# Optimization experiments

Hardware: AMD Instinct MI355X
Metric: run time of the kernel (lower is better)

Reference implementation:

```python
import jax, jax.numpy as jnp
import numpy as np

TEMPERATURE = 0.5
SCALE_BY_TEMPERATURE = True
CURV = 0.05

N = 8192
D = 128
N_PRIMARY = 32
N_SECONDARY = 16


def setup_inputs() -> dict:
    key = jax.random.key(0)
    k1, k2, k3 = jax.random.split(key, 3)
    features = jax.random.normal(k1, (N, D), dtype=jnp.float32)
    primary_labels = jax.random.randint(k2, (N,), 0, N_PRIMARY)
    secondary_labels = jax.random.randint(k3, (N,), 0, N_SECONDARY)
    return {"features": features, "primary_labels": primary_labels,
            "secondary_labels": secondary_labels}


def _hyp_contrastive_loss(features, primary_labels, secondary_labels):
    c = CURV
    sqrt_c = c ** 0.5
    n = features.shape[0]

    # L2 normalize (torch F.normalize with eps=1e-12)
    nrm = jnp.maximum(jnp.linalg.norm(features, axis=1, keepdims=True), 1e-12)
    f = features / nrm

    # Pairwise mobius_add(-f[j], f[i]) at [i, j]. With x = -f[j], y = f[i]:
    #   num = (1 + 2c<x,y> + c|y|^2) x + (1 - c|x|^2) y,   den = 1 + 2c<x,y> + c^2|x|^2|y|^2
    # We only need ||num||/den, so expand ||num||^2 algebraically to avoid an
    # [N, N, D] intermediate (same math, exact).
    n2 = jnp.sum(f * f, axis=1)            # [N], ~1 after normalize
    s = f @ f.T                            # [N, N] <f_i, f_j>
    xy = -s                                # <x, y>
    x2 = n2[None, :]                       # |x|^2 = |f_j|^2
    y2 = n2[:, None]                       # |y|^2 = |f_i|^2

    A = 1.0 + 2.0 * c * xy + c * y2
    B = 1.0 - c * x2
    den = jnp.maximum(1.0 + 2.0 * c * xy + c * c * x2 * y2, 1e-15)
    num_sq = jnp.maximum(A * A * x2 + 2.0 * A * B * xy + B * B * y2, 0.0)
    norm_diff = sqrt_c * jnp.sqrt(num_sq) / den           # [N, N]

    # artanh with clamp (pm.artanh clamps argument below 1)
    distance = jnp.arctanh(jnp.clip(norm_diff, 0.0, 1.0 - 1e-7)) * 2.0 / sqrt_c

    anchor_dot_contrast = -distance / TEMPERATURE
    logits_max = jax.lax.stop_gradient(
        jnp.max(anchor_dot_contrast, axis=1, keepdims=True))
    logits = anchor_dot_contrast - logits_max
    exp_logits = jnp.exp(logits)

    pmask = (primary_labels[:, None] == primary_labels[None, :]).astype(f.dtype)
    smask = (secondary_labels[:, None] == secondary_labels[None, :]).astype(f.dtype)
    combined = jnp.minimum(pmask + smask, 1.0)

    eye = jnp.eye(n, dtype=f.dtype)
    positives_mask = combined * (1.0 - eye)
    negatives_mask = 1.0 - combined

    num_pos = jnp.sum(positives_mask, axis=1)             # [N]
    valid = num_pos > 0

    pos_contrib = jnp.sum(exp_logits * positives_mask, axis=1)
    neg_contrib = jnp.sum(exp_logits * negatives_mask, axis=1)
    denominator = pos_contrib + neg_contrib + 1e-8        # [N]

    log_probs = logits - jnp.log(denominator)[:, None]
    row_sum = jnp.sum(log_probs * positives_mask, axis=1)
    per_row = jnp.where(valid, row_sum / jnp.maximum(num_pos, 1.0), 0.0)

    n_valid = jnp.sum(valid.astype(f.dtype))
    loss = -jnp.sum(per_row) / jnp.maximum(n_valid, 1.0)  # mean over valid rows
    loss = jnp.where(n_valid > 0, loss, 0.0)
    if SCALE_BY_TEMPERATURE:
        loss = loss * TEMPERATURE
    return jnp.nan_to_num(loss, nan=0.0, posinf=0.0, neginf=0.0)


def reference(features, primary_labels, secondary_labels):
    return _hyp_contrastive_loss(features, primary_labels, secondary_labels)
```

## Files before the change

### kernel.cpp

```cpp
#include <hip/hip_runtime.h>
#include <hip/hip_bf16.h>

#define NN 8192
#define DD 128

typedef short short8 __attribute__((ext_vector_type(8)));
typedef __bf16 bf16x8 __attribute__((ext_vector_type(8)));
typedef float f32x4 __attribute__((ext_vector_type(4)));
typedef float f32x2 __attribute__((ext_vector_type(2)));

#define MKc (-0.110803324099723f)
#define PKc (0.110803324099723f)
#define C1Kc (1.110803324099723f)
#define KEc (-8.944271909999159f)
#define KLc (-6.199696797323639f)

__global__ __launch_bounds__(256) void prep_kernel(const float* __restrict__ x,
                                                   __hip_bfloat16* __restrict__ fb,
                                                   float* __restrict__ totg,
                                                   float* __restrict__ tposg) {
  int r = threadIdx.x >> 4, sub = threadIdx.x & 15;
  int row = blockIdx.x * 16 + r;
  const float4 a = *(const float4*)(x + (size_t)row * DD + sub * 8);
  const float4 b = *(const float4*)(x + (size_t)row * DD + sub * 8 + 4);
  float ss = a.x * a.x + a.y * a.y + a.z * a.z + a.w * a.w +
             b.x * b.x + b.y * b.y + b.z * b.z + b.w * b.w;
  for (int off = 1; off < 16; off <<= 1) ss += __shfl_xor(ss, off, 16);
  float inv = 1.0f / fmaxf(sqrtf(ss), 1e-12f);
  float va[8] = {a.x, a.y, a.z, a.w, b.x, b.y, b.z, b.w};
  short8 h;
  for (int j = 0; j < 8; j++) {
    __hip_bfloat16 t = __float2bfloat16(va[j] * inv);
    h[j] = __builtin_bit_cast(short, t);
  }
  *(short8*)((short*)fb + (size_t)row * DD + sub * 8) = h;
  if (threadIdx.x < 16) {
    totg[blockIdx.x * 16 + threadIdx.x] = 0.f;
    tposg[blockIdx.x * 16 + threadIdx.x] = 0.f;
  }
}

__global__ __launch_bounds__(256, 2) void fused_kernel(
    const __hip_bfloat16* __restrict__ fbg,
    const int* __restrict__ plab, const int* __restrict__ slab,
    float* __restrict__ totg, float* __restrict__ tposg) {
  __shared__ int plc[512], slc[512];
  __shared__ float colT_l[4 * 512];
  __shared__ float colG_l[4 * 512];

  const int tid = threadIdx.x;
  const int w = tid >> 6;
  const int lane = tid & 63;
  const int lrow = lane & 15;
  const int quad = lane >> 4;

  int J = 0, rem = blockIdx.x;
  while (rem >= 64 - 4 * J) { rem -= 64 - 4 * J; J++; }
  const int I = 4 * J + rem;
  const bool needMask = (I < 4 * J + 4);
  const int R0 = I * 128;
  const int C0 = J * 512;

  for (int i = tid; i < 512; i += 256) {
    plc[i] = plab[C0 + i];
    slc[i] = slab[C0 + i];
  }
  for (int i = lane; i < 512; i += 64) {
    colT_l[w * 512 + i] = 0.f;
    colG_l[w * 512 + i] = 0.f;
  }

  bf16x8 af[2][4];
  int plr[2][4], slr[2][4];
  for (int strip = 0; strip < 2; strip++) {
    const short* fa = (const short*)fbg + (size_t)(R0 + w * 32 + strip * 16 + lrow) * DD;
    for (int kk = 0; kk < 4; kk++)
      af[strip][kk] = __builtin_bit_cast(bf16x8, *(const short8*)(fa + kk * 32 + quad * 8));
    for (int r = 0; r < 4; r++) {
      int rowg = R0 + w * 32 + strip * 16 + quad * 4 + r;
      plr[strip][r] = plab[rowg];
      slr[strip][r] = slab[rowg];
    }
  }
  __syncthreads();

  const f32x2 MK2 = {MKc, MKc}, PK2 = {PKc, PKc}, C1K2 = {C1Kc, C1Kc};
  const f32x2 KE2 = {KEc, KEc}, ZERO2 = {0.f, 0.f}, EPS2 = {1e-30f, 1e-30f};
  const f32x2 ONE2 = {1.f, 1.f};

  f32x2 t2[2][2], g2[2][2];
  for (int s_ = 0; s_ < 2; s_++)
    for (int p = 0; p < 2; p++) { t2[s_][p] = ZERO2; g2[s_][p] = ZERO2; }

  const short* bp = (const short*)fbg + (size_t)(C0 + lrow) * DD + quad * 8;
  int colg = C0 + lrow;

  for (int ct = 0; ct < 32; ct++) {
    bf16x8 bf[4];
    for (int kk = 0; kk < 4; kk++)
      bf[kk] = __builtin_bit_cast(bf16x8, *(const short8*)(bp + kk * 32));
    bp += 16 * DD;

    f32x4 acc[2];
    for (int strip = 0; strip < 2; strip++) {
      f32x4 a0 = {0.f, 0.f, 0.f, 0.f};
      for (int kk = 0; kk < 4; kk++)
        a0 = __builtin_amdgcn_mfma_f32_16x16x32_bf16(af[strip][kk], bf[kk], a0, 0, 0, 0);
      acc[strip] = a0;
    }

    const int lc = ct * 16 + lrow;
    const int pc = plc[lc];
    const int sc = slc[lc];

    f32x2 colE = ZERO2, colL = ZERO2;

    for (int strip = 0; strip < 2; strip++) {
      for (int p = 0; p < 2; p++) {
        f32x2 s2 = {acc[strip][2 * p], acc[strip][2 * p + 1]};
        f32x2 tK = __builtin_elementwise_fma(s2, MK2, PK2);
        tK = __builtin_elementwise_max(tK, ZERO2);
        f32x2 dk = __builtin_elementwise_fma(s2, MK2, C1K2);
        f32x2 m = __builtin_elementwise_max(tK * dk, EPS2);
        f32x2 rq = {__builtin_amdgcn_rsqf(m.x), __builtin_amdgcn_rsqf(m.y)};
        f32x2 nd = tK * rq;
        f32x2 p1 = nd + ONE2;
        f32x2 rr = p1 * p1 * dk;
        f32x2 lg = {__log2f(rr.x), __log2f(rr.y)};
        f32x2 el = KE2 * lg;
        f32x2 e = {exp2f(el.x), exp2f(el.y)};
        const int r0 = 2 * p, r1 = 2 * p + 1;
        bool same0 = (pc == plr[strip][r0]) || (sc == slr[strip][r0]);
        bool same1 = (pc == plr[strip][r1]) || (sc == slr[strip][r1]);
        f32x2 em, lm;
        if (needMask) {
          int rg0 = R0 + w * 32 + strip * 16 + quad * 4 + r0;
          bool ok0 = (colg < rg0);
          bool ok1 = (colg < rg0 + 1);
          em.x = ok0 ? e.x : 0.f;
          em.y = ok1 ? e.y : 0.f;
          lm.x = (same0 && ok0) ? lg.x : 0.f;
          lm.y = (same1 && ok1) ? lg.y : 0.f;
        } else {
          em = e;
          lm.x = same0 ? lg.x : 0.f;
          lm.y = same1 ? lg.y : 0.f;
        }
        t2[strip][p] += em;
        g2[strip][p] += lm;
        colE += em;
        colL += lm;
      }
    }

    float cE = colE.x + colE.y;
    float cL = colL.x + colL.y;
    cE += __shfl_xor(cE, 16, 64);
    cE += __shfl_xor(cE, 32, 64);
    cL += __shfl_xor(cL, 16, 64);
    cL += __shfl_xor(cL, 32, 64);
    if (quad == 0) {
      colT_l[w * 512 + lc] += cE;
      colG_l[w * 512 + lc] += cL;
    }
    colg += 16;
  }

  for (int strip = 0; strip < 2; strip++) {
    for (int r = 0; r < 4; r++) {
      float t = t2[strip][r >> 1][r & 1];
      float g = g2[strip][r >> 1][r & 1];
      for (int off = 1; off < 16; off <<= 1) {
        t += __shfl_xor(t, off, 16);
        g += __shfl_xor(g, off, 16);
      }
      if (lrow == 0) {
        int rowg = R0 + w * 32 + strip * 16 + quad * 4 + r;
        atomicAdd(&totg[rowg], t);
        atomicAdd(&tposg[rowg], g);
      }
    }
  }

  __syncthreads();
  for (int i = tid; i < 512; i += 256) {
    float sE = colT_l[i] + colT_l[512 + i] + colT_l[1024 + i] + colT_l[1536 + i];
    float sL = colG_l[i] + colG_l[512 + i] + colG_l[1024 + i] + colG_l[1536 + i];
    atomicAdd(&totg[C0 + i], sE);
    atomicAdd(&tposg[C0 + i], sL);
  }
}

__global__ __launch_bounds__(1024) void finalize_k(const float* __restrict__ totg,
                                                   const float* __restrict__ tposg,
                                                   const int* __restrict__ plab,
                                                   const int* __restrict__ slab,
                                                   float* __restrict__ out) {
  __shared__ int hist[512];
  __shared__ int cntP[32], cntS[16];
  __shared__ float redP[16], redV[16];
  const int tid = threadIdx.x;
  if (tid < 512) hist[tid] = 0;
  __syncthreads();
  for (int i = tid; i < NN; i += 1024)
    atomicAdd(&hist[plab[i] * 16 + slab[i]], 1);
  __syncthreads();
  if (tid < 32) {
    int s = 0;
    for (int j = 0; j < 16; j++) s += hist[tid * 16 + j];
    cntP[tid] = s;
  } else if (tid >= 64 && tid < 80) {
    int s = 0;
    for (int j = 0; j < 32; j++) s += hist[j * 16 + (tid - 64)];
    cntS[tid - 64] = s;
  }
  __syncthreads();
  float accP = 0.f, accV = 0.f;
  for (int i = tid; i < NN; i += 1024) {
    int pl = plab[i], sl = slab[i];
    int np = cntP[pl] + cntS[sl] - hist[pl * 16 + sl] - 1;
    if (np > 0) {
      accP += (KLc * tposg[i]) / (float)np - __logf(totg[i] + 1e-8f);
      accV += 1.f;
    }
  }
  for (int off = 32; off; off >>= 1) {
    accP += __shfl_xor(accP, off, 64);
    accV += __shfl_xor(accV, off, 64);
  }
  int wv = tid >> 6;
  if ((tid & 63) == 0) { redP[wv] = accP; redV[wv] = accV; }
  __syncthreads();
  if (tid == 0) {
    float sp = 0.f, sv = 0.f;
    for (int j = 0; j < 16; j++) { sp += redP[j]; sv += redV[j]; }
    float loss = -(sp / fmaxf(sv, 1.0f)) * 0.5f;
    if (sv <= 0.0f || !__builtin_isfinite(loss)) loss = 0.0f;
    out[0] = loss;
  }
}

extern "C" void kernel_launch(void* const* d_in, const int* in_sizes, int n_in,
                              void* d_out, int out_size, void* d_ws, size_t ws_size,
                              hipStream_t stream) {
  const float* x = (const float*)d_in[0];
  const int* pl = (const int*)d_in[1];
  const int* sl = (const int*)d_in[2];
  char* ws = (char*)d_ws;
  __hip_bfloat16* fb = (__hip_bfloat16*)ws;
  float* totg = (float*)(ws + 2097152);
  float* tposg = (float*)(ws + 2129920);

  prep_kernel<<<NN / 16, 256, 0, stream>>>(x, fb, totg, tposg);
  fused_kernel<<<544, 256, 0, stream>>>(fb, pl, sl, totg, tposg);
  finalize_k<<<1, 1024, 0, stream>>>(totg, tposg, pl, sl, (float*)d_out);
}
```

Before: 123.8 us.

## Balance triangular work by pairing row blocks u and 63-u across 512 blocks

Replaces the 544-block triangular tile schedule with 512 blocks. Each block handles an equal share (32 or 33 column tiles) of a paired row-block set (u and 63-u), split into up to two segments with per-tile diagonal masking. This is meant to even out per-block work and remove the tail caused by uneven triangular blocks. In exchange, labels are now read from global memory per column tile instead of from a shared-memory cache, and the per-tile mask check and segment bookkeeping add overhead.

```diff
diff --git a/kernel.cpp b/kernel.cpp
--- a/kernel.cpp
+++ b/kernel.cpp
@@ -44,9 +44,8 @@
     const __hip_bfloat16* __restrict__ fbg,
     const int* __restrict__ plab, const int* __restrict__ slab,
     float* __restrict__ totg, float* __restrict__ tposg) {
-  __shared__ int plc[512], slc[512];
-  __shared__ float colT_l[4 * 512];
-  __shared__ float colG_l[4 * 512];
+  __shared__ float colT_l[4 * 528];
+  __shared__ float colG_l[4 * 528];
 
   const int tid = threadIdx.x;
   const int w = tid >> 6;
@@ -54,140 +53,155 @@
   const int lrow = lane & 15;
   const int quad = lane >> 4;
 
-  int J = 0, rem = blockIdx.x;
-  while (rem >= 64 - 4 * J) { rem -= 64 - 4 * J; J++; }
-  const int I = 4 * J + rem;
-  const bool needMask = (I < 4 * J + 4);
-  const int R0 = I * 128;
-  const int C0 = J * 512;
-
-  for (int i = tid; i < 512; i += 256) {
-    plc[i] = plab[C0 + i];
-    slc[i] = slab[C0 + i];
-  }
-  for (int i = lane; i < 512; i += 64) {
-    colT_l[w * 512 + i] = 0.f;
-    colG_l[w * 512 + i] = 0.f;
-  }
-
-  bf16x8 af[2][4];
-  int plr[2][4], slr[2][4];
-  for (int strip = 0; strip < 2; strip++) {
-    const short* fa = (const short*)fbg + (size_t)(R0 + w * 32 + strip * 16 + lrow) * DD;
-    for (int kk = 0; kk < 4; kk++)
-      af[strip][kk] = __builtin_bit_cast(bf16x8, *(const short8*)(fa + kk * 32 + quad * 8));
-    for (int r = 0; r < 4; r++) {
-      int rowg = R0 + w * 32 + strip * 16 + quad * 4 + r;
-      plr[strip][r] = plab[rowg];
-      slr[strip][r] = slab[rowg];
-    }
-  }
-  __syncthreads();
+  const int u = blockIdx.x >> 4;
+  const int k = blockIdx.x & 15;
+  const int s = (k < 8) ? 33 * k : 32 * k + 8;
+  const int c = (k < 8) ? 33 : 32;
+  const int B = 8 * (u + 1);
+
+  const int aEnd = min(s + c, B);
+  const int aCnt = max(0, aEnd - s);
+  const int bStart = max(s, B);
+  const int bCnt = max(0, s + c - bStart);
+  int segR0[2], segCol[2], segCnt[2], segLds[2];
+  segR0[0] = 128 * u;        segCol[0] = s * 16;              segCnt[0] = aCnt; segLds[0] = 0;
+  segR0[1] = 128 * (63 - u); segCol[1] = (bStart - B) * 16;   segCnt[1] = bCnt; segLds[1] = aCnt;
+
+  for (int i = lane; i < 528; i += 64) {
+    colT_l[w * 528 + i] = 0.f;
+    colG_l[w * 528 + i] = 0.f;
+  }
 
   const f32x2 MK2 = {MKc, MKc}, PK2 = {PKc, PKc}, C1K2 = {C1Kc, C1Kc};
   const f32x2 KE2 = {KEc, KEc}, ZERO2 = {0.f, 0.f}, EPS2 = {1e-30f, 1e-30f};
   const f32x2 ONE2 = {1.f, 1.f};
 
-  f32x2 t2[2][2], g2[2][2];
-  for (int s_ = 0; s_ < 2; s_++)
-    for (int p = 0; p < 2; p++) { t2[s_][p] = ZERO2; g2[s_][p] = ZERO2; }
-
-  const short* bp = (const short*)fbg + (size_t)(C0 + lrow) * DD + quad * 8;
-  int colg = C0 + lrow;
-
-  for (int ct = 0; ct < 32; ct++) {
-    bf16x8 bf[4];
-    for (int kk = 0; kk < 4; kk++)
-      bf[kk] = __builtin_bit_cast(bf16x8, *(const short8*)(bp + kk * 32));
-    bp += 16 * DD;
-
-    f32x4 acc[2];
+  for (int seg = 0; seg < 2; seg++) {
+    const int cnt = segCnt[seg];
+    if (cnt == 0) continue;
+    const int R0 = segR0[seg];
+    const int colBase = segCol[seg];
+    const int ldsBase = segLds[seg];
+
+    bf16x8 af[2][4];
+    int plr[2][4], slr[2][4];
     for (int strip = 0; strip < 2; strip++) {
-      f32x4 a0 = {0.f, 0.f, 0.f, 0.f};
+      const short* fa = (const short*)fbg + (size_t)(R0 + w * 32 + strip * 16 + lrow) * DD;
       for (int kk = 0; kk < 4; kk++)
-        a0 = __builtin_amdgcn_mfma_f32_16x16x32_bf16(af[strip][kk], bf[kk], a0, 0, 0, 0);
-      acc[strip] = a0;
-    }
-
-    const int lc = ct * 16 + lrow;
-    const int pc = plc[lc];
-    const int sc = slc[lc];
-
-    f32x2 colE = ZERO2, colL = ZERO2;
+        af[strip][kk] = __builtin_bit_cast(bf16x8, *(const short8*)(fa + kk * 32 + quad * 8));
+      for (int r = 0; r < 4; r++) {
+        int rowg = R0 + w * 32 + strip * 16 + quad * 4 + r;
+        plr[strip][r] = plab[rowg];
+        slr[strip][r] = slab[rowg];
+      }
+    }
+
+    f32x2 t2[2][2], g2[2][2];
+    for (int s_ = 0; s_ < 2; s_++)
+      for (int p = 0; p < 2; p++) { t2[s_][p] = ZERO2; g2[s_][p] = ZERO2; }
+
+    const short* bp = (const short*)fbg + (size_t)(colBase + lrow) * DD + quad * 8;
+    int colg = colBase + lrow;
+
+    for (int ct = 0; ct < cnt; ct++) {
+      bf16x8 bf[4];
+      for (int kk = 0; kk < 4; kk++)
+        bf[kk] = __builtin_bit_cast(bf16x8, *(const short8*)(bp + kk * 32));
+      bp += 16 * DD;
+
+      f32x4 acc[2];
+      for (int strip = 0; strip < 2; strip++) {
+        f32x4 a0 = {0.f, 0.f, 0.f, 0.f};
+        for (int kk = 0; kk < 4; kk++)
+          a0 = __builtin_amdgcn_mfma_f32_16x16x32_bf16(af[strip][kk], bf[kk], a0, 0, 0, 0);
+        acc[strip] = a0;
+      }
+
+      const int pc = plab[colg];
+      const int sc = slab[colg];
+      const bool mct = (colg - lrow + 240 >= R0);
+      f32x2 colE = ZERO2, colL = ZERO2;
+
+      for (int strip = 0; strip < 2; strip++) {
+        for (int p = 0; p < 2; p++) {
+          f32x2 s2 = {acc[strip][2 * p], acc[strip][2 * p + 1]};
+          f32x2 tK = __builtin_elementwise_fma(s2, MK2, PK2);
+          tK = __builtin_elementwise_max(tK, ZERO2);
+          f32x2 dk = __builtin_elementwise_fma(s2, MK2, C1K2);
+          f32x2 m = __builtin_elementwise_max(tK * dk, EPS2);
+          f32x2 rq = {__builtin_amdgcn_rsqf(m.x), __builtin_amdgcn_rsqf(m.y)};
+          f32x2 nd = tK * rq;
+          f32x2 p1 = nd + ONE2;
+          f32x2 rr = p1 * p1 * dk;
+          f32x2 lg = {__log2f(rr.x), __log2f(rr.y)};
+          f32x2 el = KE2 * lg;
+          f32x2 e = {exp2f(el.x), exp2f(el.y)};
+          const int r0 = 2 * p, r1 = 2 * p + 1;
+          bool same0 = (pc == plr[strip][r0]) || (sc == slr[strip][r0]);
+          bool same1 = (pc == plr[strip][r1]) || (sc == slr[strip][r1]);
+          f32x2 em, lm;
+          if (mct) {
+            int rg0 = R0 + w * 32 + strip * 16 + quad * 4 + r0;
+            bool ok0 = (colg < rg0);
+            bool ok1 = (colg < rg0 + 1);
+            em.x = ok0 ? e.x : 0.f;
+            em.y = ok1 ? e.y : 0.f;
+            lm.x = (same0 && ok0) ? lg.x : 0.f;
+            lm.y = (same1 && ok1) ? lg.y : 0.f;
+          } else {
+            em = e;
+            lm.x = same0 ? lg.x : 0.f;
+            lm.y = same1 ? lg.y : 0.f;
+          }
+          t2[strip][p] += em;
+          g2[strip][p] += lm;
+          colE += em;
+          colL += lm;
+        }
+      }
+
+      float cE = colE.x + colE.y;
+      float cL = colL.x + colL.y;
+      cE += __shfl_xor(cE, 16, 64);
+      cE += __shfl_xor(cE, 32, 64);
+      cL += __shfl_xor(cL, 16, 64);
+      cL += __shfl_xor(cL, 32, 64);
+      if (quad == 0) {
+        colT_l[w * 528 + (ldsBase + ct) * 16 + lrow] += cE;
+        colG_l[w * 528 + (ldsBase + ct) * 16 + lrow] += cL;
+      }
+      colg += 16;
+    }
 
     for (int strip = 0; strip < 2; strip++) {
-      for (int p = 0; p < 2; p++) {
-        f32x2 s2 = {acc[strip][2 * p], acc[strip][2 * p + 1]};
-        f32x2 tK = __builtin_elementwise_fma(s2, MK2, PK2);
-        tK = __builtin_elementwise_max(tK, ZERO2);
-        f32x2 dk = __builtin_elementwise_fma(s2, MK2, C1K2);
-        f32x2 m = __builtin_elementwise_max(tK * dk, EPS2);
-        f32x2 rq = {__builtin_amdgcn_rsqf(m.x), __builtin_amdgcn_rsqf(m.y)};
-        f32x2 nd = tK * rq;
-        f32x2 p1 = nd + ONE2;
-        f32x2 rr = p1 * p1 * dk;
-        f32x2 lg = {__log2f(rr.x), __log2f(rr.y)};
-        f32x2 el = KE2 * lg;
-        f32x2 e = {exp2f(el.x), exp2f(el.y)};
-        const int r0 = 2 * p, r1 = 2 * p + 1;
-        bool same0 = (pc == plr[strip][r0]) || (sc == slr[strip][r0]);
-        bool same1 = (pc == plr[strip][r1]) || (sc == slr[strip][r1]);
-        f32x2 em, lm;
-        if (needMask) {
-          int rg0 = R0 + w * 32 + strip * 16 + quad * 4 + r0;
-          bool ok0 = (colg < rg0);
-          bool ok1 = (colg < rg0 + 1);
-          em.x = ok0 ? e.x : 0.f;
-          em.y = ok1 ? e.y : 0.f;
-          lm.x = (same0 && ok0) ? lg.x : 0.f;
-          lm.y = (same1 && ok1) ? lg.y : 0.f;
-        } else {
-          em = e;
-          lm.x = same0 ? lg.x : 0.f;
-          lm.y = same1 ? lg.y : 0.f;
+      for (int r = 0; r < 4; r++) {
+        float t = t2[strip][r >> 1][r & 1];
+        float g = g2[strip][r >> 1][r & 1];
+        for (int off = 1; off < 16; off <<= 1) {
+          t += __shfl_xor(t, off, 16);
+          g += __shfl_xor(g, off, 16);
         }
-        t2[strip][p] += em;
-        g2[strip][p] += lm;
-        colE += em;
-        colL += lm;
-      }
-    }
-
-    float cE = colE.x + colE.y;
-    float cL = colL.x + colL.y;
-    cE += __shfl_xor(cE, 16, 64);
-    cE += __shfl_xor(cE, 32, 64);
-    cL += __shfl_xor(cL, 16, 64);
-    cL += __shfl_xor(cL, 32, 64);
-    if (quad == 0) {
-      colT_l[w * 512 + lc] += cE;
-      colG_l[w * 512 + lc] += cL;
-    }
-    colg += 16;
-  }
-
-  for (int strip = 0; strip < 2; strip++) {
-    for (int r = 0; r < 4; r++) {
-      float t = t2[strip][r >> 1][r & 1];
-      float g = g2[strip][r >> 1][r & 1];
-      for (int off = 1; off < 16; off <<= 1) {
-        t += __shfl_xor(t, off, 16);
-        g += __shfl_xor(g, off, 16);
-      }
-      if (lrow == 0) {
-        int rowg = R0 + w * 32 + strip * 16 + quad * 4 + r;
-        atomicAdd(&totg[rowg], t);
-        atomicAdd(&tposg[rowg], g);
-      }
-    }
-  }
-
-  __syncthreads();
-  for (int i = tid; i < 512; i += 256) {
-    float sE = colT_l[i] + colT_l[512 + i] + colT_l[1024 + i] + colT_l[1536 + i];
-    float sL = colG_l[i] + colG_l[512 + i] + colG_l[1024 + i] + colG_l[1536 + i];
-    atomicAdd(&totg[C0 + i], sE);
-    atomicAdd(&tposg[C0 + i], sL);
+        if (lrow == 0) {
+          int rowg = R0 + w * 32 + strip * 16 + quad * 4 + r;
+          atomicAdd(&totg[rowg], t);
+          atomicAdd(&tposg[rowg], g);
+        }
+      }
+    }
+  }
+
+  __syncthreads();
+  const int total = (aCnt + bCnt) * 16;
+  for (int i = tid; i < total; i += 256) {
+    const int ct = i >> 4;
+    const int cin = i & 15;
+    int col;
+    if (ct < aCnt) col = segCol[0] + (ct - segLds[0]) * 16 + cin;
+    else col = segCol[1] + (ct - segLds[1]) * 16 + cin;
+    float sE = colT_l[i] + colT_l[528 + i] + colT_l[1056 + i] + colT_l[1584 + i];
+    float sL = colG_l[i] + colG_l[528 + i] + colG_l[1056 + i] + colG_l[1584 + i];
+    atomicAdd(&totg[col], sE);
+    atomicAdd(&tposg[col], sL);
   }
 }
 
@@ -252,6 +266,6 @@
   float* tposg = (float*)(ws + 2129920);
 
   prep_kernel<<<NN / 16, 256, 0, stream>>>(x, fb, totg, tposg);
-  fused_kernel<<<544, 256, 0, stream>>>(fb, pl, sl, totg, tposg);
+  fused_kernel<<<512, 256, 0, stream>>>(fb, pl, sl, totg, tposg);
   finalize_k<<<1, 1024, 0, stream>>>(totg, tposg, pl, sl, (float*)d_out);
 }
```

New measurement: 114.9 us. 1.08x faster.
